# Kernel optimization log

Hardware: AMD Instinct MI355X
Metric: run time of the kernel (lower is better)

The kernel has to match this reference:

```python
import jax, jax.numpy as jnp
import numpy as np

BATCH = 2048
NUM_UNITS = 4096
MAX_ITER = 100


def setup_inputs() -> dict:
    key = jax.random.key(0)
    k1, k2 = jax.random.split(key)
    # Initial corrupted states: binary +/-1 patterns (sign of gaussian)
    corrupted = jnp.sign(jax.random.normal(k1, (BATCH, NUM_UNITS), dtype=jnp.float32))
    corrupted = jnp.where(corrupted == 0, 1.0, corrupted)
    # Hebbian-style weight matrix stand-in: symmetric, zero diagonal
    W = jax.random.normal(k2, (NUM_UNITS, NUM_UNITS), dtype=jnp.float32)
    W = 0.5 * (W + W.T)
    W = W * (1.0 - jnp.eye(NUM_UNITS, dtype=jnp.float32))
    return {"corrupted_patterns": corrupted, "weights": W, "max_iter": MAX_ITER}


def reference(corrupted_patterns, weights, max_iter):
    def step(patterns, _):
        r = jnp.sign(patterns @ weights)          # [B, N]
        r = jnp.where(r == 0, 1.0, r)             # sign==0 -> +1, as in torch code
        return r, None

    out, _ = jax.lax.scan(step, corrupted_patterns, None, length=max_iter)
    return out
```

## Files before the change

### kernel.cpp

```cpp
#include <hip/hip_runtime.h>
#include <stdint.h>

#define NU 4096
#define NB 2048
#define KK2 8192
#define ITERS 100
#define CAP 262144
#define THETA 0.05f
#define KC 512
#define S1 0.03937007874f
#define S2 (S1 / 254.0f)

#define OFF_BT   0u
#define OFF_A0   67108864u
#define OFF_A1   83886080u
#define OFF_SUS  100663296u
#define OFF_CNT  102760448u
#define REQ_WS   102761472u

#define NT 64

typedef int i32x4 __attribute__((ext_vector_type(4)));

__device__ __forceinline__ void gl16(const void* g, void* l) {
  __builtin_amdgcn_global_load_lds(
      (const __attribute__((address_space(1))) unsigned int*)g,
      (__attribute__((address_space(3))) unsigned int*)l, 16, 0, 0);
}

__global__ void fill_kernel(float* __restrict__ out, float v) {
  int t = blockIdx.x * blockDim.x + threadIdx.x;
  int base = t << 3;
  float4 a = make_float4(v, v, v, v);
  *(float4*)(out + base) = a;
  *(float4*)(out + base + 4) = a;
}

__device__ __forceinline__ int q127(float x, float s) {
  int v = (int)rintf(x / s);
  return v < -127 ? -127 : (v > 127 ? 127 : v);
}

__global__ void decompose_kernel(const float* __restrict__ W,
                                 signed char* __restrict__ Bt) {
  int t = blockIdx.x * blockDim.x + threadIdx.x;
  int base = t << 2;
  int j = base >> 12;
  int k = base & 4095;
  float4 w = *(const float4*)(W + (size_t)j * NU + k);
  int a0 = q127(w.x, S1), a1 = q127(w.y, S1), a2 = q127(w.z, S1), a3 = q127(w.w, S1);
  float r0 = w.x - (float)a0 * S1, r1 = w.y - (float)a1 * S1;
  float r2 = w.z - (float)a2 * S1, r3 = w.w - (float)a3 * S1;
  int b0 = q127(r0, S2), b1 = q127(r1, S2), b2 = q127(r2, S2), b3 = q127(r3, S2);
  uchar4 p1 = make_uchar4((unsigned char)a0, (unsigned char)a1,
                          (unsigned char)a2, (unsigned char)a3);
  uchar4 p2 = make_uchar4((unsigned char)b0, (unsigned char)b1,
                          (unsigned char)b2, (unsigned char)b3);
  *(uchar4*)(Bt + (size_t)j * KK2 + k) = p1;
  *(uchar4*)(Bt + (size_t)j * KK2 + 4096 + k) = p2;
}

__global__ void init_kernel(const float* __restrict__ P,
                            signed char* __restrict__ A0) {
  int t = blockIdx.x * blockDim.x + threadIdx.x;
  int base = t << 3;
  float4 a = *(const float4*)(P + base);
  float4 b = *(const float4*)(P + base + 4);
  float hv[8] = {a.x, a.y, a.z, a.w, b.x, b.y, b.z, b.w};
  unsigned char s[8];
#pragma unroll
  for (int i = 0; i < 8; ++i) s[i] = (hv[i] >= 0.0f) ? 0x01u : 0xFFu;
  uint2 pk;
  pk.x = (unsigned)s[0] | ((unsigned)s[1] << 8) | ((unsigned)s[2] << 16) |
         ((unsigned)s[3] << 24);
  pk.y = (unsigned)s[4] | ((unsigned)s[5] << 8) | ((unsigned)s[6] << 16) |
         ((unsigned)s[7] << 24);
  *(uint2*)(A0 + base) = pk;
}

__global__ void emit_kernel(const signed char* __restrict__ A,
                            float* __restrict__ out) {
  int t = blockIdx.x * blockDim.x + threadIdx.x;
  int base = t << 3;
  uint2 pk = *(const uint2*)(A + base);
  float4 o0, o1;
  o0.x = (pk.x & 0x80u) ? -1.0f : 1.0f;
  o0.y = (pk.x & 0x8000u) ? -1.0f : 1.0f;
  o0.z = (pk.x & 0x800000u) ? -1.0f : 1.0f;
  o0.w = (pk.x & 0x80000000u) ? -1.0f : 1.0f;
  o1.x = (pk.y & 0x80u) ? -1.0f : 1.0f;
  o1.y = (pk.y & 0x8000u) ? -1.0f : 1.0f;
  o1.z = (pk.y & 0x800000u) ? -1.0f : 1.0f;
  o1.w = (pk.y & 0x80000000u) ? -1.0f : 1.0f;
  *(float4*)(out + base) = o0;
  *(float4*)(out + base + 4) = o1;
}

#define SCB() __builtin_amdgcn_sched_barrier(0)
#define BAR() do { __builtin_amdgcn_sched_barrier(0);          \
                   __builtin_amdgcn_s_barrier();               \
                   __builtin_amdgcn_sched_barrier(0); } while (0)
#define VMW(N) do { asm volatile("s_waitcnt vmcnt(" #N ")" ::: "memory"); \
                    __builtin_amdgcn_sched_barrier(0); } while (0)
#define MMX(AF, BF, ACC)                                                      \
  _Pragma("unroll") for (int i_ = 0; i_ < 4; ++i_)                            \
  _Pragma("unroll") for (int j_ = 0; j_ < 4; ++j_)                            \
    ACC[i_][j_] = __builtin_amdgcn_mfma_i32_16x16x64_i8(                      \
        AF[i_], BF[j_], ACC[i_][j_], 0, 0, 0);
#define RD4S(DST, BASE) _Pragma("unroll")                                     \
  for (int q_ = 0; q_ < 4; ++q_)                                              \
    DST[q_] = *(const i32x4*)((BASE) + q_ * 1024);

#define TB(k, CFa, CFh, CFl, PFa, PFh, PFl)                                   \
  {                                                                           \
    const int kS_ = ((k) + 4) << 6;                                           \
    SCB();                                                                    \
    MMX(CFa, CFh, acc1);                           \
    SCB();                                                                    \
    if ((k) + 1 < NT) {                                                       \
      RD4S(PFa, sp1 + aOff);                                                  \
      RD4S(PFh, sp1 + 16384 + bOff);                                          \
    }                                                                         \
    if ((k) + 4 < NT) {                                                       \
      gl16(pAs + kS_, sp4 + ldsA);                                            \
      gl16(pAs2 + kS_, sp4 + ldsA + 1024);                                    \
    }                                                                         \
    SCB();                                                                    \
    MMX(CFa, CFl, acc2);                           \
    SCB();                                                                    \
    if ((k) + 1 < NT) { RD4S(PFl, sp1 + 24576 + bOff); }                      \
    if ((k) + 4 < NT) {                                                       \
      gl16(pBsH + kS_, sp4 + 16384 + ldsB);                                   \
      gl16(pBsL + kS_, sp4 + 24576 + ldsB);                                   \
    }                                                                         \
    SCB();                                                                    \
    if ((k) < NT - 4) { VMW(8); }                                             \
    else if ((k) == NT - 4) { VMW(4); }                                       \
    else { VMW(0); }                                                          \
    BAR();                                                                    \
    unsigned char* r_ = sp0;                                                  \
    sp0 = sp1; sp1 = sp2; sp2 = sp3; sp3 = sp4; sp4 = r_;                     \
  }

__global__ void __launch_bounds__(512, 1)
gemm_fused_kernel(const signed char* __restrict__ A,
                  const signed char* __restrict__ Bt,
                  signed char* __restrict__ Anext,
                  int* __restrict__ counter,
                  int* __restrict__ suspects) {
  __shared__ __align__(16) unsigned char sL[163840];
  const int tid = threadIdx.x;
  const int wave = tid >> 6, lane = tid & 63;
  const int lm = lane & 15, lk = lane >> 4;
  const int wm = wave >> 1, wn = wave & 1;
  const int nt = blockIdx.x & 31, mt = blockIdx.x >> 5;
  const int mBase = mt << 8, nBase = nt << 7;

  const int rl = lane >> 2;
  const int cs = ((((lane & 3) - ((lane >> 3) & 3)) & 3) << 4);
  const signed char* pAs = A + (size_t)(mBase + (wave << 5) + rl) * NU + cs;
  const signed char* pAs2 = pAs + (size_t)16 * NU;
  const signed char* pBsH = Bt + (size_t)(nBase + (wave << 4) + rl) * KK2 + cs;
  const signed char* pBsL = pBsH + 4096;
  const int ldsA = wave << 11;
  const int ldsB = wave << 10;
  unsigned char* sp0 = sL;
  unsigned char* sp1 = sL + 32768;
  unsigned char* sp2 = sL + 65536;
  unsigned char* sp3 = sL + 98304;
  unsigned char* sp4 = sL + 131072;

  const int pslot = (lk + ((lm >> 1) & 3)) & 3;
  const int aOff = (((wm << 6) + lm) << 6) + (pslot << 4);
  const int bOff = (((wn << 6) + lm) << 6) + (pslot << 4);

  i32x4 acc1[4][4] = {};
  i32x4 acc2[4][4] = {};
  i32x4 afA[4], bhA[4], blA[4], afB[4], bhB[4], blB[4];

  gl16(pAs, sp0 + ldsA);           gl16(pAs2, sp0 + ldsA + 1024);
  gl16(pBsH, sp0 + 16384 + ldsB);  gl16(pBsL, sp0 + 24576 + ldsB);
  gl16(pAs + 64, sp1 + ldsA);          gl16(pAs2 + 64, sp1 + ldsA + 1024);
  gl16(pBsH + 64, sp1 + 16384 + ldsB); gl16(pBsL + 64, sp1 + 24576 + ldsB);
  gl16(pAs + 128, sp2 + ldsA);          gl16(pAs2 + 128, sp2 + ldsA + 1024);
  gl16(pBsH + 128, sp2 + 16384 + ldsB); gl16(pBsL + 128, sp2 + 24576 + ldsB);
  gl16(pAs + 192, sp3 + ldsA);          gl16(pAs2 + 192, sp3 + ldsA + 1024);
  gl16(pBsH + 192, sp3 + 16384 + ldsB); gl16(pBsL + 192, sp3 + 24576 + ldsB);
  VMW(0);
  BAR();
  RD4S(afA, sp0 + aOff);
  RD4S(bhA, sp0 + 16384 + bOff);
  RD4S(blA, sp0 + 24576 + bOff);

  for (int k = 0; k < NT; k += 2) {
    TB(k + 0, afA, bhA, blA, afB, bhB, blB);
    TB(k + 1, afB, bhB, blB, afA, bhA, blA);
  }

#pragma unroll
  for (int i = 0; i < 4; ++i)
#pragma unroll
    for (int j = 0; j < 4; ++j)
#pragma unroll
      for (int r = 0; r < 4; ++r) {
        const int row = mBase + (wm << 6) + i * 16 + (lk << 2) + r;
        const int col = nBase + (wn << 6) + j * 16 + lm;
        const float h = S1 * (float)acc1[i][j][r] + S2 * (float)acc2[i][j][r];
        Anext[(size_t)row * NU + col] =
            (h >= 0.0f) ? (signed char)1 : (signed char)-1;
        if (fabsf(h) < THETA) {
          int sidx = atomicAdd(counter, 1);
          if (sidx < CAP) suspects[sidx] = (row << 12) | col;
        }
      }
}

__global__ void fixup_kernel(const signed char* __restrict__ Acur,
                             const float* __restrict__ W,
                             signed char* __restrict__ Anext,
                             const int* __restrict__ counter,
                             const int* __restrict__ suspects,
                             int* __restrict__ flagOv) {
  int n = *counter;
  if (blockIdx.x == 0 && threadIdx.x == 0 && n > CAP) atomicAdd(flagOv, 1);
  n = n < CAP ? n : CAP;
  const int lane = threadIdx.x & 7;
  const int gid = (blockIdx.x * blockDim.x + threadIdx.x) >> 3;
  const int ngrp = (gridDim.x * blockDim.x) >> 3;
  for (int i = gid; i < n; i += ngrp) {
    int idx = suspects[i];
    int b = idx >> 12, j = idx & 4095;
    const float* wrow = W + (size_t)j * NU + lane * KC;
    const signed char* arow = Acur + (size_t)b * NU + lane * KC;
    float part = 0.0f;
    for (int k = 0; k < KC; k += 4) {
      float4 wv = *(const float4*)(wrow + k);
      unsigned av = *(const unsigned*)(arow + k);
      part += (av & 0x80u) ? -wv.x : wv.x;
      part += (av & 0x8000u) ? -wv.y : wv.y;
      part += (av & 0x800000u) ? -wv.z : wv.z;
      part += (av & 0x80000000u) ? -wv.w : wv.w;
    }
    float c = __shfl(part, 0, 8);
#pragma unroll
    for (int q = 1; q < 8; ++q) c += __shfl(part, q, 8);
    if (lane == 0) {
      Anext[(size_t)b * NU + j] = (c >= 0.0f) ? (signed char)1 : (signed char)-1;
    }
  }
}

__global__ void assemble_kernel(float* __restrict__ out,
                                const int* __restrict__ flags) {
  if (threadIdx.x != 0 || blockIdx.x != 0) return;
  if (flags[1]) out[0] = 7777.0f;
}

extern "C" void kernel_launch(void* const* d_in, const int* in_sizes, int n_in,
                              void* d_out, int out_size, void* d_ws, size_t ws_size,
                              hipStream_t stream) {
  const float* P = (const float*)d_in[0];
  const float* W = (const float*)d_in[1];
  float* out = (float*)d_out;

  if (n_in < 2 || in_sizes[0] != NB * NU || in_sizes[1] != NU * NU ||
      out_size != NB * NU) {
    fill_kernel<<<4096, 256, 0, stream>>>(out, 9.0f);
    return;
  }
  if (ws_size < (size_t)REQ_WS) {
    fill_kernel<<<4096, 256, 0, stream>>>(out, 3.0f);
    return;
  }

  char* w = (char*)d_ws;
  signed char* Bt = (signed char*)(w + OFF_BT);
  signed char* A0 = (signed char*)(w + OFF_A0);
  signed char* A1 = (signed char*)(w + OFF_A1);
  int* suspects = (int*)(w + OFF_SUS);
  int* counters = (int*)(w + OFF_CNT);
  int* flags = counters + 128;

  hipMemsetAsync(counters, 0, 1024, stream);
  decompose_kernel<<<16384, 256, 0, stream>>>(W, Bt);
  init_kernel<<<4096, 256, 0, stream>>>(P, A0);

  for (int t = 0; t < ITERS; ++t) {
    signed char* Ain = (t & 1) ? A1 : A0;
    signed char* Aout = (t & 1) ? A0 : A1;
    gemm_fused_kernel<<<256, 512, 0, stream>>>(Ain, Bt, Aout,
                                               &counters[t], suspects);
    fixup_kernel<<<256, 256, 0, stream>>>(Ain, W, Aout,
                                          &counters[t], suspects, &flags[1]);
  }
  emit_kernel<<<4096, 256, 0, stream>>>(A0, out);
  assemble_kernel<<<1, 64, 0, stream>>>(out, flags);
}
```

Baseline: 9.118 ms.

## Store activations in MFMA-fragment tiled layout and load A directly to registers

Activation matrices are now kept in a tiled layout that matches the MFMA A-fragment order, so each wave loads its A fragments straight from global memory into registers with dwordx4 loads instead of staging them through LDS. The LDS ring now holds only the B high/low tiles, giving an 8-slot ring with deeper prefetch and a smaller LDS footprint. Init, emit, the epilogue store and the fixup kernel are updated to the new addressing. This removes the LDS traffic and barrier pressure for A, but the direct global loads must now be hidden by the register pipeline, and the scattered byte stores in the epilogue may coalesce less well.

```diff
diff --git a/kernel.cpp b/kernel.cpp
--- a/kernel.cpp
+++ b/kernel.cpp
@@ -26,6 +26,12 @@
   __builtin_amdgcn_global_load_lds(
       (const __attribute__((address_space(1))) unsigned int*)g,
       (__attribute__((address_space(3))) unsigned int*)l, 16, 0, 0);
+}
+
+__device__ __forceinline__ i32x4 ald(const signed char* p) {
+  i32x4 r;
+  asm volatile("global_load_dwordx4 %0, %1, off" : "=v"(r) : "v"(p));
+  return r;
 }
 
 __global__ void fill_kernel(float* __restrict__ out, float v) {
@@ -63,26 +69,35 @@
 __global__ void init_kernel(const float* __restrict__ P,
                             signed char* __restrict__ A0) {
   int t = blockIdx.x * blockDim.x + threadIdx.x;
-  int base = t << 3;
-  float4 a = *(const float4*)(P + base);
-  float4 b = *(const float4*)(P + base + 4);
-  float hv[8] = {a.x, a.y, a.z, a.w, b.x, b.y, b.z, b.w};
-  unsigned char s[8];
-#pragma unroll
-  for (int i = 0; i < 8; ++i) s[i] = (hv[i] >= 0.0f) ? 0x01u : 0xFFu;
-  uint2 pk;
-  pk.x = (unsigned)s[0] | ((unsigned)s[1] << 8) | ((unsigned)s[2] << 16) |
-         ((unsigned)s[3] << 24);
-  pk.y = (unsigned)s[4] | ((unsigned)s[5] << 8) | ((unsigned)s[6] << 16) |
-         ((unsigned)s[7] << 24);
-  *(uint2*)(A0 + base) = pk;
+  int row = t >> 8, kc = t & 255;
+  const float4* p = (const float4*)(P + (size_t)row * NU + (kc << 4));
+  float4 v0 = p[0], v1 = p[1], v2 = p[2], v3 = p[3];
+  float hv[16] = {v0.x, v0.y, v0.z, v0.w, v1.x, v1.y, v1.z, v1.w,
+                  v2.x, v2.y, v2.z, v2.w, v3.x, v3.y, v3.z, v3.w};
+  unsigned un[4];
+#pragma unroll
+  for (int g = 0; g < 4; ++g) {
+    unsigned u = 0;
+#pragma unroll
+    for (int i = 0; i < 4; ++i) {
+      unsigned char s = (hv[g * 4 + i] >= 0.0f) ? 0x01u : 0xFFu;
+      u |= ((unsigned)s) << (i * 8);
+    }
+    un[g] = u;
+  }
+  uint4 pk = make_uint4(un[0], un[1], un[2], un[3]);
+  size_t addr = ((size_t)(kc >> 2) << 17) + ((size_t)(row >> 4) << 10) +
+                ((row & 15) << 4) + ((kc & 3) << 8);
+  *(uint4*)(A0 + addr) = pk;
 }
 
 __global__ void emit_kernel(const signed char* __restrict__ A,
                             float* __restrict__ out) {
   int t = blockIdx.x * blockDim.x + threadIdx.x;
-  int base = t << 3;
-  uint2 pk = *(const uint2*)(A + base);
+  int row = t >> 9, k8 = (t & 511) << 3;
+  size_t addr = ((size_t)(k8 >> 6) << 17) + ((size_t)(row >> 4) << 10) +
+                ((row & 15) << 4) + (((k8 >> 4) & 3) << 8) + (k8 & 15);
+  uint2 pk = *(const uint2*)(A + addr);
   float4 o0, o1;
   o0.x = (pk.x & 0x80u) ? -1.0f : 1.0f;
   o0.y = (pk.x & 0x8000u) ? -1.0f : 1.0f;
@@ -92,8 +107,8 @@
   o1.y = (pk.y & 0x8000u) ? -1.0f : 1.0f;
   o1.z = (pk.y & 0x800000u) ? -1.0f : 1.0f;
   o1.w = (pk.y & 0x80000000u) ? -1.0f : 1.0f;
-  *(float4*)(out + base) = o0;
-  *(float4*)(out + base + 4) = o1;
+  *(float4*)(out + (size_t)row * NU + k8) = o0;
+  *(float4*)(out + (size_t)row * NU + k8 + 4) = o1;
 }
 
 #define SCB() __builtin_amdgcn_sched_barrier(0)
@@ -111,35 +126,62 @@
   for (int q_ = 0; q_ < 4; ++q_)                                              \
     DST[q_] = *(const i32x4*)((BASE) + q_ * 1024);
 
-#define TB(k, CFa, CFh, CFl, PFa, PFh, PFl)                                   \
+#define APRIME(PA, kt)                                                        \
   {                                                                           \
-    const int kS_ = ((k) + 4) << 6;                                           \
-    SCB();                                                                    \
-    MMX(CFa, CFh, acc1);                           \
-    SCB();                                                                    \
+    const signed char* pa_ = pA0 + ((size_t)(kt) << 17);                      \
+    PA[0] = ald(pa_);          PA[1] = ald(pa_ + 1024);                       \
+    PA[2] = ald(pa_ + 2048);   PA[3] = ald(pa_ + 3072);                       \
+  }
+
+#define TBF(k, CA, PA, CH, PH)                                                \
+  {                                                                           \
+    SCB();                                                                    \
+    MMX(CA, CH, acc1);                                                        \
+    SCB();                                                                    \
+    RD4S(bl, sL + (((k) & 7) << 14) + 8192 + bOff);                           \
+    SCB();                                                                    \
+    APRIME(PA, (k) + 2);                                                      \
+    SCB();                                                                    \
+    {                                                                         \
+      const int kS_ = ((k) + 6) << 6;                                         \
+      unsigned char* sS_ = sL + ((((k) + 6) & 7) << 14);                      \
+      gl16(pBsH + kS_, sS_ + ldsB);                                           \
+      gl16(pBsL + kS_, sS_ + 8192 + ldsB);                                    \
+    }                                                                         \
+    RD4S(PH, sL + ((((k) + 1) & 7) << 14) + bOff);                            \
+    SCB();                                                                    \
+    MMX(CA, bl, acc2);                                                        \
+    SCB();                                                                    \
+    VMW(8);                                                                   \
+    BAR();                                                                    \
+  }
+
+#define TBT(k, CA, PA, CH, PH)                                                \
+  {                                                                           \
+    SCB();                                                                    \
+    MMX(CA, CH, acc1);                                                        \
+    SCB();                                                                    \
+    RD4S(bl, sL + (((k) & 7) << 14) + 8192 + bOff);                           \
+    SCB();                                                                    \
+    if ((k) + 2 < NT) { APRIME(PA, (k) + 2); }                                \
+    SCB();                                                                    \
+    if ((k) + 6 < NT) {                                                       \
+      const int kS_ = ((k) + 6) << 6;                                         \
+      unsigned char* sS_ = sL + ((((k) + 6) & 7) << 14);                      \
+      gl16(pBsH + kS_, sS_ + ldsB);                                           \
+      gl16(pBsL + kS_, sS_ + 8192 + ldsB);                                    \
+    }                                                                         \
     if ((k) + 1 < NT) {                                                       \
-      RD4S(PFa, sp1 + aOff);                                                  \
-      RD4S(PFh, sp1 + 16384 + bOff);                                          \
+      RD4S(PH, sL + ((((k) + 1) & 7) << 14) + bOff);                          \
     }                                                                         \
-    if ((k) + 4 < NT) {                                                       \
-      gl16(pAs + kS_, sp4 + ldsA);                                            \
-      gl16(pAs2 + kS_, sp4 + ldsA + 1024);                                    \
-    }                                                                         \
-    SCB();                                                                    \
-    MMX(CFa, CFl, acc2);                           \
-    SCB();                                                                    \
-    if ((k) + 1 < NT) { RD4S(PFl, sp1 + 24576 + bOff); }                      \
-    if ((k) + 4 < NT) {                                                       \
-      gl16(pBsH + kS_, sp4 + 16384 + ldsB);                                   \
-      gl16(pBsL + kS_, sp4 + 24576 + ldsB);                                   \
-    }                                                                         \
-    SCB();                                                                    \
-    if ((k) < NT - 4) { VMW(8); }                                             \
-    else if ((k) == NT - 4) { VMW(4); }                                       \
+    SCB();                                                                    \
+    MMX(CA, bl, acc2);                                                        \
+    SCB();                                                                    \
+    if ((k) <= NT - 7) { VMW(8); }                                            \
+    else if ((k) == NT - 6) { VMW(6); }                                       \
+    else if ((k) <= NT - 3) { VMW(4); }                                       \
     else { VMW(0); }                                                          \
     BAR();                                                                    \
-    unsigned char* r_ = sp0;                                                  \
-    sp0 = sp1; sp1 = sp2; sp2 = sp3; sp3 = sp4; sp4 = r_;                     \
   }
 
 __global__ void __launch_bounds__(512, 1)
@@ -148,7 +190,7 @@
                   signed char* __restrict__ Anext,
                   int* __restrict__ counter,
                   int* __restrict__ suspects) {
-  __shared__ __align__(16) unsigned char sL[163840];
+  __shared__ __align__(16) unsigned char sL[131072];
   const int tid = threadIdx.x;
   const int wave = tid >> 6, lane = tid & 63;
   const int lm = lane & 15, lk = lane >> 4;
@@ -156,46 +198,51 @@
   const int nt = blockIdx.x & 31, mt = blockIdx.x >> 5;
   const int mBase = mt << 8, nBase = nt << 7;
 
+  const signed char* pA0 =
+      A + (((size_t)(mt * 16 + wm * 4)) << 10) + (lane << 4);
+
   const int rl = lane >> 2;
   const int cs = ((((lane & 3) - ((lane >> 3) & 3)) & 3) << 4);
-  const signed char* pAs = A + (size_t)(mBase + (wave << 5) + rl) * NU + cs;
-  const signed char* pAs2 = pAs + (size_t)16 * NU;
   const signed char* pBsH = Bt + (size_t)(nBase + (wave << 4) + rl) * KK2 + cs;
   const signed char* pBsL = pBsH + 4096;
-  const int ldsA = wave << 11;
   const int ldsB = wave << 10;
-  unsigned char* sp0 = sL;
-  unsigned char* sp1 = sL + 32768;
-  unsigned char* sp2 = sL + 65536;
-  unsigned char* sp3 = sL + 98304;
-  unsigned char* sp4 = sL + 131072;
 
   const int pslot = (lk + ((lm >> 1) & 3)) & 3;
-  const int aOff = (((wm << 6) + lm) << 6) + (pslot << 4);
   const int bOff = (((wn << 6) + lm) << 6) + (pslot << 4);
 
   i32x4 acc1[4][4] = {};
   i32x4 acc2[4][4] = {};
-  i32x4 afA[4], bhA[4], blA[4], afB[4], bhB[4], blB[4];
-
-  gl16(pAs, sp0 + ldsA);           gl16(pAs2, sp0 + ldsA + 1024);
-  gl16(pBsH, sp0 + 16384 + ldsB);  gl16(pBsL, sp0 + 24576 + ldsB);
-  gl16(pAs + 64, sp1 + ldsA);          gl16(pAs2 + 64, sp1 + ldsA + 1024);
-  gl16(pBsH + 64, sp1 + 16384 + ldsB); gl16(pBsL + 64, sp1 + 24576 + ldsB);
-  gl16(pAs + 128, sp2 + ldsA);          gl16(pAs2 + 128, sp2 + ldsA + 1024);
-  gl16(pBsH + 128, sp2 + 16384 + ldsB); gl16(pBsL + 128, sp2 + 24576 + ldsB);
-  gl16(pAs + 192, sp3 + ldsA);          gl16(pAs2 + 192, sp3 + ldsA + 1024);
-  gl16(pBsH + 192, sp3 + 16384 + ldsB); gl16(pBsL + 192, sp3 + 24576 + ldsB);
+  i32x4 a0[4], a1[4], a2[4], h0[4], h1[4], bl[4];
+
+#pragma unroll
+  for (int j = 0; j < 6; ++j) {
+    gl16(pBsH + (j << 6), sL + (j << 14) + ldsB);
+    gl16(pBsL + (j << 6), sL + (j << 14) + 8192 + ldsB);
+  }
+  APRIME(a0, 0);
+  APRIME(a1, 1);
   VMW(0);
   BAR();
-  RD4S(afA, sp0 + aOff);
-  RD4S(bhA, sp0 + 16384 + bOff);
-  RD4S(blA, sp0 + 24576 + bOff);
-
-  for (int k = 0; k < NT; k += 2) {
-    TB(k + 0, afA, bhA, blA, afB, bhB, blB);
-    TB(k + 1, afB, bhB, blB, afA, bhA, blA);
-  }
+  RD4S(h0, sL + bOff);
+
+  for (int k = 0; k < 54; k += 6) {
+    TBF(k + 0, a0, a2, h0, h1);
+    TBF(k + 1, a1, a0, h1, h0);
+    TBF(k + 2, a2, a1, h0, h1);
+    TBF(k + 3, a0, a2, h1, h0);
+    TBF(k + 4, a1, a0, h0, h1);
+    TBF(k + 5, a2, a1, h1, h0);
+  }
+  TBT(54, a0, a2, h0, h1);
+  TBT(55, a1, a0, h1, h0);
+  TBT(56, a2, a1, h0, h1);
+  TBT(57, a0, a2, h1, h0);
+  TBT(58, a1, a0, h0, h1);
+  TBT(59, a2, a1, h1, h0);
+  TBT(60, a0, a2, h0, h1);
+  TBT(61, a1, a0, h1, h0);
+  TBT(62, a2, a1, h0, h1);
+  TBT(63, a0, a2, h1, h0);
 
 #pragma unroll
   for (int i = 0; i < 4; ++i)
@@ -206,8 +253,10 @@
         const int row = mBase + (wm << 6) + i * 16 + (lk << 2) + r;
         const int col = nBase + (wn << 6) + j * 16 + lm;
         const float h = S1 * (float)acc1[i][j][r] + S2 * (float)acc2[i][j][r];
-        Anext[(size_t)row * NU + col] =
-            (h >= 0.0f) ? (signed char)1 : (signed char)-1;
+        const size_t taddr = ((size_t)(col >> 6) << 17) +
+                             ((size_t)(row >> 4) << 10) + ((row & 15) << 4) +
+                             (((col >> 4) & 3) << 8) + (col & 15);
+        Anext[taddr] = (h >= 0.0f) ? (signed char)1 : (signed char)-1;
         if (fabsf(h) < THETA) {
           int sidx = atomicAdd(counter, 1);
           if (sidx < CAP) suspects[sidx] = (row << 12) | col;
@@ -230,12 +279,15 @@
   for (int i = gid; i < n; i += ngrp) {
     int idx = suspects[i];
     int b = idx >> 12, j = idx & 4095;
-    const float* wrow = W + (size_t)j * NU + lane * KC;
-    const signed char* arow = Acur + (size_t)b * NU + lane * KC;
+    const float* wrow = W + (size_t)j * NU;
+    const size_t baseb = ((size_t)(b >> 4) << 10) + ((b & 15) << 4);
     float part = 0.0f;
-    for (int k = 0; k < KC; k += 4) {
+    const int k0 = lane * KC;
+    for (int k = k0; k < k0 + KC; k += 4) {
       float4 wv = *(const float4*)(wrow + k);
-      unsigned av = *(const unsigned*)(arow + k);
+      unsigned av = *(const unsigned*)(Acur + (((size_t)(k >> 6)) << 17) +
+                                       baseb + (((k >> 4) & 3) << 8) +
+                                       (k & 15));
       part += (av & 0x80u) ? -wv.x : wv.x;
       part += (av & 0x8000u) ? -wv.y : wv.y;
       part += (av & 0x800000u) ? -wv.z : wv.z;
@@ -245,7 +297,10 @@
 #pragma unroll
     for (int q = 1; q < 8; ++q) c += __shfl(part, q, 8);
     if (lane == 0) {
-      Anext[(size_t)b * NU + j] = (c >= 0.0f) ? (signed char)1 : (signed char)-1;
+      const size_t taddr = ((size_t)(j >> 6) << 17) +
+                           ((size_t)(b >> 4) << 10) + ((b & 15) << 4) +
+                           (((j >> 4) & 3) << 8) + (j & 15);
+      Anext[taddr] = (c >= 0.0f) ? (signed char)1 : (signed char)-1;
     }
   }
 }
@@ -283,7 +338,7 @@
 
   hipMemsetAsync(counters, 0, 1024, stream);
   decompose_kernel<<<16384, 256, 0, stream>>>(W, Bt);
-  init_kernel<<<4096, 256, 0, stream>>>(P, A0);
+  init_kernel<<<2048, 256, 0, stream>>>(P, A0);
 
   for (int t = 0; t < ITERS; ++t) {
     signed char* Ain = (t & 1) ? A1 : A0;
```

Result: slower. 9.735 ms (+6.8%).
